# Performance work log

Measured on AMD Instinct MI355X. Metric: run time of the kernel, lower is better.

Reference implementation:

```python
import jax, jax.numpy as jnp
import numpy as np

BATCH, NUM_BSS, NUM_USERS, M, N = 32, 8, 32, 128, 4
LAGR_ITERS = 8
PSEUDOINV_SVAL_THRESH = 1e-12


def herm(a):
    return 0.5 * (a + jnp.swapaxes(a, -1, -2).conj())


def setup_inputs() -> dict:
    key = jax.random.key(0)
    ks = jax.random.split(key, 7)
    v_re = jax.random.normal(ks[0], (BATCH, NUM_USERS, M, N), jnp.float32)
    v_im = jax.random.normal(ks[1], (BATCH, NUM_USERS, M, N), jnp.float32)
    H_re = jax.random.normal(ks[2], (NUM_BSS, NUM_USERS, N, M), jnp.float32)
    H_im = jax.random.normal(ks[3], (NUM_BSS, NUM_USERS, N, M), jnp.float32)
    noise_pow = jax.random.uniform(ks[4], (BATCH, NUM_USERS), jnp.float32, 0.05, 1.0)
    rweights = jax.random.uniform(ks[5], (BATCH, NUM_USERS), jnp.float32, 0.1, 1.0)
    bss_pow = jnp.ones((BATCH, NUM_BSS), jnp.float32)
    assign = jax.random.randint(ks[6], (NUM_USERS,), 0, NUM_BSS).astype(jnp.int32)
    return {"v_re": v_re, "v_im": v_im, "H_re": H_re, "H_im": H_im,
            "noise_pow": noise_pow, "rweights": rweights, "bss_pow": bss_pow,
            "assign": assign}


def reference(v_re, v_im, H_re, H_im, noise_pow, rweights, bss_pow, assign):
    V = v_re + 1j * v_im          # [B,K,M,N] precoders
    H = H_re + 1j * H_im          # [C,K,N,M] channel BS c -> user k
    K = V.shape[1]
    C = H.shape[0]
    Ndim = V.shape[-1]
    eyeN = jnp.eye(Ndim, dtype=V.dtype)

    # Hg[j, i] = channel from assigned-BS-of-user-j to user i
    Hg = H[assign]                                    # [K,K,N,M]
    # downlink covariance per user i: noise*I + sum_j (H[bs_j,i] V_j)(.)^H
    HV = jnp.einsum('jinm,bjmp->bijnp', Hg, V)        # [B,Ki,Kj,N,N]
    cov = jnp.einsum('bijnp,bijqp->binq', HV, HV.conj())
    cov = herm(cov + noise_pow[..., None, None] * eyeN)
    icov = herm(jnp.linalg.inv(cov))                  # [B,K,N,N]

    idx = jnp.arange(K)
    Hd = Hg[idx, idx]                                 # [K,N,M] direct channels
    HdV = jnp.einsum('knm,bkmp->bknp', Hd, V)         # [B,K,N,N]
    u = jnp.einsum('bknq,bkqp->bknp', icov, HdV)      # receive filters
    w_inv = herm(eyeN - jnp.einsum('bkqn,bkqp->bknp', u.conj(), HdV))
    w = herm(jnp.linalg.inv(w_inv))                   # MSE weights (w_poly=None)
    uwu = herm(jnp.einsum('bknp,bkpq,bkrq->bknr', u, w, u.conj()))
    # v_tilde = H_ii^H u w * rate_weight
    vt = jnp.einsum('knm,bknp,bkpq->bkmq', Hd.conj(), u, w) * rweights[..., None, None]

    # uplink covariance per BS c: sum_k rw_k * H[c,k]^H uwu_k H[c,k]
    ul = herm(jnp.einsum('cknm,bkno,ckop,bk->bcmp', H.conj(), uwu, H, rweights))

    # aux per BS: sum over assigned users of v_tilde v_tilde^H
    Q = jnp.einsum('bkmn,bkpn->bkmp', vt, vt.conj())  # [B,K,M,M]
    aux = jnp.moveaxis(
        jax.ops.segment_sum(jnp.moveaxis(Q, 1, 0), assign, num_segments=C), 0, 1)  # [B,C,M,M]

    lam, E = jnp.linalg.eigh(ul)                      # [B,C,M], [B,C,M,M]
    lam = jnp.maximum(lam, 0.0)
    c = jnp.maximum(jnp.einsum('bcmi,bcmp,bcpi->bci', E.conj(), aux, E).real, 0.0)
    c = c / bss_pow[..., None]

    # solve sum_i c_i/(lam_i+mu)^2 = 1 for mu >= 0 by bisection in [0, sqrt(sum c)]
    hi = jnp.sqrt(jnp.sum(c, -1))
    lo = jnp.zeros_like(hi)
    for _ in range(LAGR_ITERS):
        mid = 0.5 * (lo + hi)
        f = jnp.sum(c / jnp.square(lam + mid[..., None] + 1e-20), -1)
        gt = f > 1.0
        lo = jnp.where(gt, mid, lo)
        hi = jnp.where(gt, hi, mid)
    mu = jnp.maximum(0.5 * (lo + hi), 0.0)            # [B,C]

    # pseudo-inverse of loaded UL covariance via its eigendecomposition
    lam_l = lam + mu[..., None]
    lam_l = jnp.where(lam_l < PSEUDOINV_SVAL_THRESH, 1e12, lam_l)
    inv_aug = herm(jnp.einsum('bcmi,bci,bcni->bcmn', E, 1.0 / lam_l, E.conj()))

    # v update: v_k = inv_aug[assign_k] @ v_tilde_k
    v_out = jnp.einsum('bkmp,bkpn->bkmn', inv_aug[:, assign], vt)  # [B,K,M,N]
    return v_out
```

## Files before the change

kernel.cpp:

```cpp
#include <hip/hip_runtime.h>

#define B_ 32
#define C_ 8
#define K_ 32
#define NCMAX 96
#define BSTR 129

__device__ __forceinline__ float2 cmul(float2 a, float2 b) {
  return make_float2(a.x*b.x - a.y*b.y, a.x*b.y + a.y*b.x);
}
__device__ __forceinline__ float2 cmulc(float2 a, float2 b) {
  return make_float2(a.x*b.x + a.y*b.y, a.y*b.x - a.x*b.y);
}
__device__ __forceinline__ float2 cadd(float2 a, float2 b){ return make_float2(a.x+b.x, a.y+b.y); }
__device__ __forceinline__ float2 csub(float2 a, float2 b){ return make_float2(a.x-b.x, a.y-b.y); }
__device__ __forceinline__ int SK(int r){ return r + ((r >> 3) << 1); }

__device__ void herm4_inv(float2 a[4][4], float2 out[4][4]) {
  float idg[4];
  for (int j = 0; j < 4; ++j) {
    float d = sqrtf(fmaxf(a[j][j].x, 1e-30f));
    float id = 1.f / d;
    idg[j] = id;
    a[j][j] = make_float2(d, 0.f);
    for (int r = j+1; r < 4; ++r) { a[r][j].x *= id; a[r][j].y *= id; }
    for (int c = j+1; c < 4; ++c)
      for (int r = c; r < 4; ++r)
        a[r][c] = csub(a[r][c], cmulc(a[r][j], a[c][j]));
  }
  float2 li[4][4];
  for (int j = 0; j < 4; ++j) {
    li[j][j] = make_float2(idg[j], 0.f);
    for (int r = j+1; r < 4; ++r) {
      float2 s = make_float2(0.f, 0.f);
      for (int d = j; d < r; ++d) s = cadd(s, cmul(a[r][d], li[d][j]));
      li[r][j] = make_float2(-s.x*idg[r], -s.y*idg[r]);
    }
  }
  for (int p = 0; p < 4; ++p)
    for (int q = 0; q < 4; ++q) {
      float2 s = make_float2(0.f, 0.f);
      for (int d = (p > q ? p : q); d < 4; ++d)
        s = cadd(s, cmulc(li[d][q], li[d][p]));
      out[p][q] = s;
    }
}

__global__ __launch_bounds__(512, 1) void k_fused(
    const float* __restrict__ v_re, const float* __restrict__ v_im,
    const float* __restrict__ H_re, const float* __restrict__ H_im,
    const float* __restrict__ noise_pow, const float* __restrict__ rweights,
    const float* __restrict__ bss_pow, const int* __restrict__ assign_g,
    void* __restrict__ outp, int omode)
{
  const int t = threadIdx.x;
  const int lane = t & 63, wid = t >> 6;
  const int blk = blockIdx.x;
  const int b = blk >> 3, c = blk & 7;
  const int tm = t >> 4, tp = t & 15;
  const int rbase = tm * 4, cbase = tp * 8;

  __shared__ __align__(16) float2 BsL[NCMAX * BSTR];
  __shared__ __align__(16) float2 Arena[4224];
  __shared__ __align__(16) float2 pS[1024];
  __shared__ __align__(16) float2 dBS2[256];
  __shared__ __align__(16) float2 wS[160];
  __shared__ __align__(16) float2 colS[160];
  __shared__ __align__(16) float2 pvS[128];
  __shared__ __align__(16) float2 tauS[128];
  __shared__ float dS[128], eS[128], cpS[128];
  __shared__ float red[8];
  __shared__ int asg[K_], ulist[K_], nc_s;

  float2* Wall = pS;
  float2* uwS  = pS + 512;
  float2* covS = Arena + 2576;
  float2* HdVS = Arena + 3088;
  float2* Pd   = Arena;
  float2* Tsc  = Arena;
  float2* Vp   = Arena;

  if (t < K_) asg[t] = assign_g[t];
  if (t == 0) {
    int n2 = 0;
    for (int k = 0; k < K_; ++k) if (assign_g[k] == c) ulist[n2++] = k;
    nc_s = n2;
  }
  {
    const int k = t >> 4, n = (t >> 2) & 3, q = t & 3;
    covS[t] = make_float2((n == q) ? noise_pow[b*K_ + k] : 0.f, 0.f);
  }
  __syncthreads();
  const int nc = nc_s;
  if (nc == 0) return;
  const int cols = 4 * nc;
  const int qmax = (cols + 15) >> 4;
  const int passes = (cols + 31) >> 5;

  {
    const int pn = t >> 2, qt = t & 3;
    const int kk = pn >> 2, nn = pn & 3;
    float2* Tb0 = Arena + 1552;
    float2* Tb1 = Arena + 2064;
    for (int j = 0; j < K_; j += 2) {
      #pragma unroll
      for (int bf = 0; bf < 2; ++bf) {
        const int vb = (b*K_ + j + bf) * 512;
        Arena[bf*776 + (t >> 2)*6 + (t & 3) + (t >> 7)*2] =
            make_float2(v_re[vb + t], v_im[vb + t]);
      }
      __syncthreads();
      float2 rr[2][4];
      #pragma unroll
      for (int bf = 0; bf < 2; ++bf) {
        const float2* Vq = Arena + bf*776 + qt*2;
        const int hb = ((asg[j + bf]*K_ + kk)*4 + nn) * 128;
        float2 a0 = {0,0}, a1 = {0,0}, a2 = {0,0}, a3 = {0,0};
        for (int m4 = qt*32; m4 < qt*32 + 32; m4 += 4) {
          const float4 hre = *(const float4*)&H_re[hb + m4];
          const float4 him = *(const float4*)&H_im[hb + m4];
          const float hx[4] = {hre.x, hre.y, hre.z, hre.w};
          const float hy[4] = {him.x, him.y, him.z, him.w};
          #pragma unroll
          for (int i2 = 0; i2 < 4; ++i2) {
            const float4 v01 = *(const float4*)&Vq[(m4 + i2)*6];
            const float4 v23 = *(const float4*)&Vq[(m4 + i2)*6 + 2];
            a0.x += hx[i2]*v01.x - hy[i2]*v01.y; a0.y += hx[i2]*v01.y + hy[i2]*v01.x;
            a1.x += hx[i2]*v01.z - hy[i2]*v01.w; a1.y += hx[i2]*v01.w + hy[i2]*v01.z;
            a2.x += hx[i2]*v23.x - hy[i2]*v23.y; a2.y += hx[i2]*v23.y + hy[i2]*v23.x;
            a3.x += hx[i2]*v23.z - hy[i2]*v23.w; a3.y += hx[i2]*v23.w + hy[i2]*v23.z;
          }
        }
        rr[bf][0] = a0; rr[bf][1] = a1; rr[bf][2] = a2; rr[bf][3] = a3;
      }
      #pragma unroll
      for (int o = 1; o <= 2; o <<= 1) {
        #pragma unroll
        for (int bf = 0; bf < 2; ++bf)
          #pragma unroll
          for (int p = 0; p < 4; ++p) {
            rr[bf][p].x += __shfl_xor(rr[bf][p].x, o, 64);
            rr[bf][p].y += __shfl_xor(rr[bf][p].y, o, 64);
          }
      }
      if (qt == 0) {
        #pragma unroll
        for (int p = 0; p < 4; ++p) {
          Tb0[pn*4 + p] = rr[0][p];
          Tb1[pn*4 + p] = rr[1][p];
        }
      }
      __syncthreads();
      {
        const int k2 = t >> 4, n2 = (t >> 2) & 3, q2 = t & 3;
        float2 acc = covS[t];
        #pragma unroll
        for (int p = 0; p < 4; ++p)
          acc = cadd(acc, cmulc(Tb0[(k2*4 + n2)*4 + p], Tb0[(k2*4 + q2)*4 + p]));
        #pragma unroll
        for (int p = 0; p < 4; ++p)
          acc = cadd(acc, cmulc(Tb1[(k2*4 + n2)*4 + p], Tb1[(k2*4 + q2)*4 + p]));
        covS[t] = acc;
        if (k2 == j)     HdVS[k2*16 + n2*4 + q2] = Tb0[(k2*4 + n2)*4 + q2];
        if (k2 == j + 1) HdVS[k2*16 + n2*4 + q2] = Tb1[(k2*4 + n2)*4 + q2];
      }
      __syncthreads();
    }
  }

  if (t < K_) {
    const int k = t;
    float2 a[4][4], ic[4][4], hv[4][4], u[4][4], wi[4][4], w[4][4], uw[4][4], W[4][4];
    const float rwk = rweights[b*K_ + k];
    for (int r = 0; r < 4; ++r)
      for (int c2 = 0; c2 < 4; ++c2) a[r][c2] = covS[k*16 + r*4 + c2];
    herm4_inv(a, ic);
    for (int r = 0; r < 4; ++r)
      for (int c2 = 0; c2 < 4; ++c2) hv[r][c2] = HdVS[k*16 + r*4 + c2];
    for (int n = 0; n < 4; ++n)
      for (int p = 0; p < 4; ++p) {
        float2 s = {0,0};
        for (int q = 0; q < 4; ++q) s = cadd(s, cmul(ic[n][q], hv[q][p]));
        u[n][p] = s;
      }
    for (int n = 0; n < 4; ++n)
      for (int p = 0; p < 4; ++p) {
        float2 s = make_float2((n == p) ? 1.f : 0.f, 0.f);
        for (int q = 0; q < 4; ++q) s = csub(s, cmulc(hv[q][p], u[q][n]));
        wi[n][p] = s;
      }
    herm4_inv(wi, w);
    for (int n = 0; n < 4; ++n)
      for (int q = 0; q < 4; ++q) {
        float2 s = {0,0};
        for (int p = 0; p < 4; ++p) s = cadd(s, cmul(u[n][p], w[p][q]));
        uw[n][q] = s;
      }
    for (int n = 0; n < 4; ++n)
      for (int r = 0; r < 4; ++r) {
        float2 s = {0,0};
        for (int q = 0; q < 4; ++q) s = cadd(s, cmulc(uw[n][q], u[r][q]));
        W[n][r] = make_float2(s.x * rwk, s.y * rwk);
      }
    for (int n = 0; n < 4; ++n)
      for (int r = n; r < 4; ++r) {
        float2 x1 = W[n][r], x2 = W[r][n];
        float2 hm = make_float2(0.5f*(x1.x + x2.x), 0.5f*(x1.y - x2.y));
        W[n][r] = hm; W[r][n] = make_float2(hm.x, -hm.y);
      }
    for (int idx = 0; idx < 16; ++idx) {
      uwS[k*16 + idx]  = uw[idx >> 2][idx & 3];
      Wall[k*16 + idx] = W[idx >> 2][idx & 3];
    }
  }
  __syncthreads();

  float2 Areg[4][8];
  #pragma unroll
  for (int j = 0; j < 4; ++j)
    #pragma unroll
    for (int cc = 0; cc < 8; ++cc) Areg[j][cc] = make_float2(0.f, 0.f);
  for (int k = 0; k < K_; k += 2) {
    #pragma unroll
    for (int bf = 0; bf < 2; ++bf) {
      const int hb = (c*K_ + k + bf) * 512;
      Arena[bf*520 + (t >> 7)*130 + (t & 127)] = make_float2(H_re[hb + t], H_im[hb + t]);
    }
    __syncthreads();
    #pragma unroll
    for (int bf = 0; bf < 2; ++bf) {
      const int n = t >> 7, p = t & 127;
      const float2* HsB = Arena + bf*520;
      const int kb = (k + bf)*16 + n*4;
      float2 y = {0,0};
      #pragma unroll
      for (int o = 0; o < 4; ++o) y = cadd(y, cmul(Wall[kb + o], HsB[o*130 + p]));
      Arena[1040 + bf*640 + n*160 + p + ((p >> 3) << 1)] = y;
    }
    __syncthreads();
    #pragma unroll
    for (int bf = 0; bf < 2; ++bf) {
      const float2* HsB = Arena + bf*520;
      const float2* YsB = Arena + 1040 + bf*640;
      #pragma unroll
      for (int n = 0; n < 4; ++n) {
        const float4 ha = *(const float4*)&HsB[n*130 + rbase];
        const float4 hc = *(const float4*)&HsB[n*130 + rbase + 2];
        const float2 h0 = make_float2(ha.x, ha.y), h1 = make_float2(ha.z, ha.w);
        const float2 h2 = make_float2(hc.x, hc.y), h3 = make_float2(hc.z, hc.w);
        const float2* yb = &YsB[n*160 + tp*10];
        #pragma unroll
        for (int hq = 0; hq < 2; ++hq) {
          float2 y[4];
          #pragma unroll
          for (int a2 = 0; a2 < 4; a2 += 2) {
            const float4 y4 = *(const float4*)&yb[hq*4 + a2];
            y[a2] = make_float2(y4.x, y4.y); y[a2+1] = make_float2(y4.z, y4.w);
          }
          #pragma unroll
          for (int c4 = 0; c4 < 4; ++c4) {
            const int cc = hq*4 + c4;
            Areg[0][cc].x += h0.x*y[c4].x + h0.y*y[c4].y;
            Areg[0][cc].y += h0.x*y[c4].y - h0.y*y[c4].x;
            Areg[1][cc].x += h1.x*y[c4].x + h1.y*y[c4].y;
            Areg[1][cc].y += h1.x*y[c4].y - h1.y*y[c4].x;
            Areg[2][cc].x += h2.x*y[c4].x + h2.y*y[c4].y;
            Areg[2][cc].y += h2.x*y[c4].y - h2.y*y[c4].x;
            Areg[3][cc].x += h3.x*y[c4].x + h3.y*y[c4].y;
            Areg[3][cc].y += h3.x*y[c4].y - h3.y*y[c4].x;
          }
        }
      }
    }
    __syncthreads();
  }

  float2 Bv[4][8];
  #pragma unroll
  for (int j = 0; j < 4; ++j)
    #pragma unroll
    for (int q = 0; q < 8; ++q) Bv[j][q] = make_float2(0.f, 0.f);
  float trp = 0.f;
  #pragma unroll
  for (int q = 0; q < 8; ++q) {
    const int col = tp + 16*q;
    const int slot = col >> 2, qn = col & 3;
    if (slot < nc) {
      const int k = ulist[slot];
      const float rwk = rweights[b*K_ + k];
      const int hb = (c*K_ + k) * 512;
      float2 acc0 = {0,0}, acc1 = {0,0}, acc2 = {0,0}, acc3 = {0,0};
      #pragma unroll
      for (int n = 0; n < 4; ++n) {
        const float2 uwv = uwS[k*16 + n*4 + qn];
        const float4 hre = *(const float4*)&H_re[hb + n*128 + rbase];
        const float4 him = *(const float4*)&H_im[hb + n*128 + rbase];
        acc0 = cadd(acc0, cmulc(uwv, make_float2(hre.x, him.x)));
        acc1 = cadd(acc1, cmulc(uwv, make_float2(hre.y, him.y)));
        acc2 = cadd(acc2, cmulc(uwv, make_float2(hre.z, him.z)));
        acc3 = cadd(acc3, cmulc(uwv, make_float2(hre.w, him.w)));
      }
      acc0.x *= rwk; acc0.y *= rwk; acc1.x *= rwk; acc1.y *= rwk;
      acc2.x *= rwk; acc2.y *= rwk; acc3.x *= rwk; acc3.y *= rwk;
      Bv[0][q] = acc0; Bv[1][q] = acc1; Bv[2][q] = acc2; Bv[3][q] = acc3;
      trp += acc0.x*acc0.x + acc0.y*acc0.y + acc1.x*acc1.x + acc1.y*acc1.y
           + acc2.x*acc2.x + acc2.y*acc2.y + acc3.x*acc3.x + acc3.y*acc3.y;
    }
  }
  #pragma unroll
  for (int o = 32; o >= 1; o >>= 1) trp += __shfl_xor(trp, o, 64);
  if (lane == 0) red[wid] = trp;
  __syncthreads();
  const float inv_bss = 1.f / bss_pow[b*C_ + c];
  float hi = sqrtf((red[0] + red[1] + red[2] + red[3] +
                    red[4] + red[5] + red[6] + red[7]) * inv_bss);
  float lo = 0.f;

  if (tp == 0) {
    #pragma unroll
    for (int j = 0; j < 4; ++j) colS[SK(rbase + j)] = Areg[j][0];
  }
  __syncthreads();

  #pragma unroll 1
  for (int i = 0; i < 127; ++i) {
    float2 vr[4], vc[8], tau, sc;
    {
      const float2 x0 = colS[SK(lane)], x1 = colS[SK(lane + 64)];
      float sig = 0.f;
      if (lane >= i + 2)      sig += x0.x*x0.x + x0.y*x0.y;
      if (lane + 64 >= i + 2) sig += x1.x*x1.x + x1.y*x1.y;
      #pragma unroll
      for (int o = 32; o >= 1; o >>= 1) sig += __shfl_xor(sig, o, 64);
      const float2 al = colS[SK(i + 1)];
      float beta;
      if (sig <= 1e-30f && fabsf(al.y) <= 1e-30f) {
        beta = al.x; tau = make_float2(0.f, 0.f); sc = make_float2(0.f, 0.f);
      } else {
        const float mag = sqrtf(al.x*al.x + al.y*al.y + sig);
        beta = (al.x >= 0.f) ? -mag : mag;
        const float ib = 1.f / beta;
        tau = make_float2((beta - al.x) * ib, -al.y * ib);
        const float dx = al.x - beta, dy = al.y;
        const float dn = 1.f / (dx*dx + dy*dy);
        sc = make_float2(dx*dn, -dy*dn);
      }
      if (t == 0) { eS[i] = beta; tauS[i] = tau; }
      #pragma unroll
      for (int j = 0; j < 4; ++j) {
        const int r = rbase + j;
        const float2 x = colS[SK(r)];
        vr[j] = (r <= i) ? make_float2(0.f, 0.f)
              : (r == i + 1 ? make_float2(1.f, 0.f) : cmul(x, sc));
      }
      {
        const int cb = SK(cbase);
        const float4 c01 = *(const float4*)&colS[cb];
        const float4 c23 = *(const float4*)&colS[cb + 2];
        const float4 c45 = *(const float4*)&colS[cb + 4];
        const float4 c67 = *(const float4*)&colS[cb + 6];
        const float2 cx[8] = { make_float2(c01.x,c01.y), make_float2(c01.z,c01.w),
                               make_float2(c23.x,c23.y), make_float2(c23.z,c23.w),
                               make_float2(c45.x,c45.y), make_float2(c45.z,c45.w),
                               make_float2(c67.x,c67.y), make_float2(c67.z,c67.w) };
        #pragma unroll
        for (int cc = 0; cc < 8; ++cc) {
          const int r = cbase + cc;
          vc[cc] = (r <= i) ? make_float2(0.f, 0.f)
                 : (r == i + 1 ? make_float2(1.f, 0.f) : cmul(cx[cc], sc));
        }
      }
    }
    {
      float2 part[4];
      #pragma unroll
      for (int j = 0; j < 4; ++j) {
        float2 s = cmul(Areg[j][0], vc[0]);
        #pragma unroll
        for (int cc = 1; cc < 8; ++cc) s = cadd(s, cmul(Areg[j][cc], vc[cc]));
        part[j] = s;
      }
      #pragma unroll
      for (int o = 1; o <= 8; o <<= 1) {
        #pragma unroll
        for (int j = 0; j < 4; ++j) {
          part[j].x += __shfl_xor(part[j].x, o, 64);
          part[j].y += __shfl_xor(part[j].y, o, 64);
        }
      }
      #pragma unroll
      for (int j = 0; j < 4; ++j) if (tp == j) pvS[rbase + j] = part[j];
      #pragma unroll
      for (int q = 0; q < 8; ++q) {
        if (q >= qmax) continue;
        float2 s = {0.f, 0.f};
        #pragma unroll
        for (int j = 0; j < 4; ++j) s = cadd(s, cmulc(Bv[j][q], vr[j]));
        Pd[tm*130 + tp + 16*q] = s;
      }
    }
    __syncthreads();

    if (wid == 0) {
      float2 p0 = {0.f,0.f}, p1 = {0.f,0.f};
      if (lane > i)      p0 = cmul(tau, pvS[lane]);
      if (lane + 64 > i) p1 = cmul(tau, pvS[lane + 64]);
      float2 v0, v1;
      v0 = (lane <= i) ? make_float2(0.f,0.f)
         : (lane == i + 1 ? make_float2(1.f,0.f) : cmul(colS[SK(lane)], sc));
      { const int r1 = lane + 64;
        v1 = (r1 <= i) ? make_float2(0.f,0.f)
           : (r1 == i + 1 ? make_float2(1.f,0.f) : cmul(colS[SK(r1)], sc)); }
      float2 d0 = cadd(cmulc(p0, v0), cmulc(p1, v1));
      #pragma unroll
      for (int o = 32; o >= 1; o >>= 1) {
        d0.x += __shfl_xor(d0.x, o, 64);
        d0.y += __shfl_xor(d0.y, o, 64);
      }
      const float alr = -0.5f * (tau.x*d0.x + tau.y*d0.y);
      wS[SK(lane)]      = cadd(p0, make_float2(alr*v0.x, alr*v0.y));
      wS[SK(lane + 64)] = cadd(p1, make_float2(alr*v1.x, alr*v1.y));
    } else if (t < 320) {
      const int col = (t - 64) & 127;
      const int half = (t - 64) >> 7;
      float2 s = {0.f, 0.f};
      #pragma unroll
      for (int g = 0; g < 16; ++g) s = cadd(s, Pd[(half*16 + g)*130 + col]);
      dBS2[half*128 + col] = s;
    }
    __syncthreads();

    {
      float2 wr[4], wc[8];
      #pragma unroll
      for (int j = 0; j < 4; ++j) wr[j] = wS[SK(rbase + j)];
      {
        const int cb = SK(cbase);
        const float4 w01 = *(const float4*)&wS[cb];
        const float4 w23 = *(const float4*)&wS[cb + 2];
        const float4 w45 = *(const float4*)&wS[cb + 4];
        const float4 w67 = *(const float4*)&wS[cb + 6];
        wc[0] = make_float2(w01.x,w01.y); wc[1] = make_float2(w01.z,w01.w);
        wc[2] = make_float2(w23.x,w23.y); wc[3] = make_float2(w23.z,w23.w);
        wc[4] = make_float2(w45.x,w45.y); wc[5] = make_float2(w45.z,w45.w);
        wc[6] = make_float2(w67.x,w67.y); wc[7] = make_float2(w67.z,w67.w);
      }
      #pragma unroll
      for (int j = 0; j < 4; ++j)
        #pragma unroll
        for (int cc = 0; cc < 8; ++cc)
          Areg[j][cc] = csub(Areg[j][cc], cadd(cmulc(vr[j], wc[cc]), cmulc(wr[j], vc[cc])));
      const float2 tauc = make_float2(tau.x, -tau.y);
      #pragma unroll
      for (int q = 0; q < 8; ++q) {
        if (q >= qmax) continue;
        const float2 dBt = cmul(tauc, cadd(dBS2[tp + 16*q], dBS2[128 + tp + 16*q]));
        #pragma unroll
        for (int j = 0; j < 4; ++j) Bv[j][q] = csub(Bv[j][q], cmul(dBt, vr[j]));
      }
      if (tp == (i >> 3)) {
        #pragma unroll
        for (int cc = 0; cc < 8; ++cc) if (cc == (i & 7)) {
          #pragma unroll
          for (int j = 0; j < 4; ++j) if (rbase + j >= i + 1) Areg[j][cc] = vr[j];
        }
      }
      if (tp == ((i + 1) >> 3)) {
        #pragma unroll
        for (int cc = 0; cc < 8; ++cc) if (cc == ((i + 1) & 7)) {
          #pragma unroll
          for (int j = 0; j < 4; ++j) colS[SK(rbase + j)] = Areg[j][cc];
        }
      }
    }
    __syncthreads();
  }

  if (tp == (tm >> 1)) {
    const int co = (tm & 1) * 4;
    #pragma unroll
    for (int j = 0; j < 4; ++j)
      #pragma unroll
      for (int cc = 0; cc < 8; ++cc)
        if (cc == co + j) dS[rbase + j] = Areg[j][cc].x;
  }
  #pragma unroll
  for (int q = 0; q < 8; ++q) {
    const int col = tp + 16*q;
    if ((col >> 2) < nc) {
      #pragma unroll
      for (int j = 0; j < 4; ++j) BsL[col*BSTR + rbase + j] = Bv[j][q];
    }
  }
  __syncthreads();

  if (wid == 0) {
    for (int it = 0; it <= 8; ++it) {
      const float mu = 0.5f * (lo + hi);
      float fsum = 0.f;
      for (int p = 0; p < passes; ++p) {
        const int colg = 32*p + (lane & 31);
        const bool act = (lane < 32) && (colg < cols);
        float2* Bcol = BsL + colg*BSTR;
        float m = dS[0] + mu;
        float im = 1.f / m;
        float2 g = act ? Bcol[0] : make_float2(0.f, 0.f);
        g.x *= im; g.y *= im;
        if (act) Tsc[lane] = g;
        float cp = eS[0] * im;
        if (lane == 0) cpS[0] = cp;
        for (int r = 1; r < 128; ++r) {
          const float e0 = eS[r-1];
          m = dS[r] + mu - e0 * cp;
          im = 1.f / m;
          float2 gr = act ? Bcol[r] : make_float2(0.f, 0.f);
          gr.x = (gr.x - e0 * g.x) * im;
          gr.y = (gr.y - e0 * g.y) * im;
          g = gr;
          if (act) Tsc[r*33 + lane] = gr;
          if (r < 127) { cp = eS[r] * im; if (lane == 0) cpS[r] = cp; }
        }
        float2 z = g;
        float acc = z.x*z.x + z.y*z.y;
        if (it == 8 && act) Bcol[127] = z;
        for (int r = 126; r >= 0; --r) {
          const float cpr = cpS[r];
          const float2 gp = act ? Tsc[r*33 + lane] : make_float2(0.f, 0.f);
          z.x = gp.x - cpr * z.x;
          z.y = gp.y - cpr * z.y;
          acc += z.x*z.x + z.y*z.y;
          if (it == 8 && act) Bcol[r] = z;
        }
        if (act) fsum += acc;
      }
      if (it < 8) {
        #pragma unroll
        for (int o = 32; o >= 1; o >>= 1) fsum += __shfl_xor(fsum, o, 64);
        const float f = fsum * inv_bss;
        if (f > 1.0f) lo = mu; else hi = mu;
      }
    }
  }
  __syncthreads();

  for (int base = 0; base < cols; base += 32) {
    float2 z0[4], z1[4];
    bool act[4];
    #pragma unroll
    for (int qq = 0; qq < 4; ++qq) {
      const int col = base + wid + 8*qq;
      act[qq] = (col < cols);
      const int cc2 = act[qq] ? col : 0;
      z0[qq] = BsL[cc2*BSTR + lane];
      z1[qq] = BsL[cc2*BSTR + lane + 64];
    }
    for (int P = 7; P >= 0; --P) {
      const int p0i = P * 16;
      const int smax = (P == 7) ? 14 : 15;
      __syncthreads();
      if (tp == 2*P) {
        #pragma unroll
        for (int s = 0; s < 8; ++s) {
          const int ii = p0i + s;
          #pragma unroll
          for (int j = 0; j < 4; ++j) {
            const int r = rbase + j;
            Vp[(s << 7) + r] = (r >= ii + 1) ? Areg[j][s] : make_float2(0.f, 0.f);
          }
        }
      }
      if (tp == 2*P + 1) {
        #pragma unroll
        for (int s = 8; s < 16; ++s) {
          if (s > smax) continue;
          const int ii = p0i + s;
          #pragma unroll
          for (int j = 0; j < 4; ++j) {
            const int r = rbase + j;
            Vp[(s << 7) + r] = (r >= ii + 1) ? Areg[j][s - 8] : make_float2(0.f, 0.f);
          }
        }
      }
      __syncthreads();
      for (int s = smax; s >= 0; --s) {
        const float2 tv = tauS[p0i + s];
        const float2 v0 = Vp[(s << 7) + lane];
        const float2 v1 = Vp[(s << 7) + lane + 64];
        float2 d[4];
        #pragma unroll
        for (int qq = 0; qq < 4; ++qq)
          d[qq] = cadd(cmulc(z0[qq], v0), cmulc(z1[qq], v1));
        #pragma unroll
        for (int o = 32; o >= 1; o >>= 1) {
          #pragma unroll
          for (int qq = 0; qq < 4; ++qq) {
            d[qq].x += __shfl_xor(d[qq].x, o, 64);
            d[qq].y += __shfl_xor(d[qq].y, o, 64);
          }
        }
        #pragma unroll
        for (int qq = 0; qq < 4; ++qq) {
          const float2 td = cmul(tv, d[qq]);
          z0[qq] = csub(z0[qq], cmul(td, v0));
          z1[qq] = csub(z1[qq], cmul(td, v1));
        }
      }
    }
    #pragma unroll
    for (int qq = 0; qq < 4; ++qq) if (act[qq]) {
      const int col = base + wid + 8*qq;
      const int slotc = col >> 2, qn = col & 3;
      const int k = ulist[slotc];
      const size_t obase = (size_t)(b*K_ + k) * 512;
      const size_t oe0 = obase + (size_t)lane*4 + qn;
      const size_t oe1 = obase + (size_t)(lane + 64)*4 + qn;
      if (omode == 0) {
        ((float2*)outp)[oe0] = z0[qq];
        ((float2*)outp)[oe1] = z1[qq];
      } else {
        ((float*)outp)[oe0] = z0[qq].x;
        ((float*)outp)[oe1] = z1[qq].x;
      }
    }
  }
}

extern "C" void kernel_launch(void* const* d_in, const int* in_sizes, int n_in,
                              void* d_out, int out_size, void* d_ws, size_t ws_size,
                              hipStream_t stream)
{
  (void)in_sizes; (void)n_in; (void)d_ws; (void)ws_size;
  const float* v_re   = (const float*)d_in[0];
  const float* v_im   = (const float*)d_in[1];
  const float* H_re   = (const float*)d_in[2];
  const float* H_im   = (const float*)d_in[3];
  const float* noise  = (const float*)d_in[4];
  const float* rw     = (const float*)d_in[5];
  const float* bss    = (const float*)d_in[6];
  const int*   assign = (const int*)d_in[7];

  const int omode = (out_size == B_*K_*128*4) ? 1 : 0;

  hipLaunchKernelGGL(k_fused, dim3(B_*C_), dim3(512), 0, stream,
                     v_re, v_im, H_re, H_im, noise, rw, bss, assign, d_out, omode);
}
```

Before: 1.354 ms.

## Defer Householder rank-2 update to next iteration, dropping one barrier per step

The Householder tridiagonalization loop is restructured so the rank-2 trailing update of the register-held matrix and the B update from step i run at the start of step i+1. The next pivot column is computed directly by wave 0 from a raw column copy plus the new v and w vectors, instead of being extracted after the full update. This removes one __syncthreads per iteration across 127 iterations. In exchange it adds a vLds buffer, a colRaw buffer and some shuffles, and the column correction must exactly match the deferred update.

```diff
diff --git a/kernel.cpp b/kernel.cpp
--- a/kernel.cpp
+++ b/kernel.cpp
@@ -65,7 +65,9 @@
   __shared__ __align__(16) float2 pS[1024];
   __shared__ __align__(16) float2 dBS2[256];
   __shared__ __align__(16) float2 wS[160];
+  __shared__ __align__(16) float2 vLds[160];
   __shared__ __align__(16) float2 colS[160];
+  __shared__ __align__(16) float2 colRaw[128];
   __shared__ __align__(16) float2 pvS[128];
   __shared__ __align__(16) float2 tauS[128];
   __shared__ float dS[128], eS[128], cpS[128];
@@ -322,8 +324,58 @@
   }
   __syncthreads();
 
+  float2 tau_p = make_float2(0.f, 0.f);
+
   #pragma unroll 1
   for (int i = 0; i < 127; ++i) {
+    if (i > 0) {
+      const int ip = i - 1;
+      float2 vr4[4], wr4[4], vc4[8], wc4[8];
+      #pragma unroll
+      for (int j = 0; j < 4; ++j) {
+        vr4[j] = vLds[SK(rbase + j)];
+        wr4[j] = wS[SK(rbase + j)];
+      }
+      {
+        const int cb = SK(cbase);
+        const float4 v01 = *(const float4*)&vLds[cb];
+        const float4 v23 = *(const float4*)&vLds[cb + 2];
+        const float4 v45 = *(const float4*)&vLds[cb + 4];
+        const float4 v67 = *(const float4*)&vLds[cb + 6];
+        vc4[0] = make_float2(v01.x,v01.y); vc4[1] = make_float2(v01.z,v01.w);
+        vc4[2] = make_float2(v23.x,v23.y); vc4[3] = make_float2(v23.z,v23.w);
+        vc4[4] = make_float2(v45.x,v45.y); vc4[5] = make_float2(v45.z,v45.w);
+        vc4[6] = make_float2(v67.x,v67.y); vc4[7] = make_float2(v67.z,v67.w);
+        const float4 w01 = *(const float4*)&wS[cb];
+        const float4 w23 = *(const float4*)&wS[cb + 2];
+        const float4 w45 = *(const float4*)&wS[cb + 4];
+        const float4 w67 = *(const float4*)&wS[cb + 6];
+        wc4[0] = make_float2(w01.x,w01.y); wc4[1] = make_float2(w01.z,w01.w);
+        wc4[2] = make_float2(w23.x,w23.y); wc4[3] = make_float2(w23.z,w23.w);
+        wc4[4] = make_float2(w45.x,w45.y); wc4[5] = make_float2(w45.z,w45.w);
+        wc4[6] = make_float2(w67.x,w67.y); wc4[7] = make_float2(w67.z,w67.w);
+      }
+      #pragma unroll
+      for (int j = 0; j < 4; ++j)
+        #pragma unroll
+        for (int cc = 0; cc < 8; ++cc)
+          Areg[j][cc] = csub(Areg[j][cc], cadd(cmulc(vr4[j], wc4[cc]), cmulc(wr4[j], vc4[cc])));
+      const float2 tauc = make_float2(tau_p.x, -tau_p.y);
+      #pragma unroll
+      for (int q = 0; q < 8; ++q) {
+        if (q >= qmax) continue;
+        const float2 dBt = cmul(tauc, cadd(dBS2[tp + 16*q], dBS2[128 + tp + 16*q]));
+        #pragma unroll
+        for (int j = 0; j < 4; ++j) Bv[j][q] = csub(Bv[j][q], cmul(dBt, vr4[j]));
+      }
+      if (tp == (ip >> 3)) {
+        #pragma unroll
+        for (int cc = 0; cc < 8; ++cc) if (cc == (ip & 7)) {
+          #pragma unroll
+          for (int j = 0; j < 4; ++j) if (rbase + j >= ip + 1) Areg[j][cc] = vr4[j];
+        }
+      }
+    }
     float2 vr[4], vc[8], tau, sc;
     {
       const float2 x0 = colS[SK(lane)], x1 = colS[SK(lane + 64)];
@@ -398,6 +450,13 @@
         for (int j = 0; j < 4; ++j) s = cadd(s, cmulc(Bv[j][q], vr[j]));
         Pd[tm*130 + tp + 16*q] = s;
       }
+      if (tp == ((i + 1) >> 3)) {
+        #pragma unroll
+        for (int cc = 0; cc < 8; ++cc) if (cc == ((i + 1) & 7)) {
+          #pragma unroll
+          for (int j = 0; j < 4; ++j) colRaw[rbase + j] = Areg[j][cc];
+        }
+      }
     }
     __syncthreads();
 
@@ -418,8 +477,19 @@
         d0.y += __shfl_xor(d0.y, o, 64);
       }
       const float alr = -0.5f * (tau.x*d0.x + tau.y*d0.y);
-      wS[SK(lane)]      = cadd(p0, make_float2(alr*v0.x, alr*v0.y));
-      wS[SK(lane + 64)] = cadd(p1, make_float2(alr*v1.x, alr*v1.y));
+      const float2 w0 = cadd(p0, make_float2(alr*v0.x, alr*v0.y));
+      const float2 w1 = cadd(p1, make_float2(alr*v1.x, alr*v1.y));
+      wS[SK(lane)]      = w0;
+      wS[SK(lane + 64)] = w1;
+      vLds[SK(lane)]      = v0;
+      vLds[SK(lane + 64)] = v1;
+      const int rs = (i + 1) & 63;
+      const float bx0 = __shfl(w0.x, rs, 64), by0 = __shfl(w0.y, rs, 64);
+      const float bx1 = __shfl(w1.x, rs, 64), by1 = __shfl(w1.y, rs, 64);
+      const float2 wb = (i + 1 < 64) ? make_float2(bx0, by0) : make_float2(bx1, by1);
+      const float2 c0 = colRaw[lane], c1 = colRaw[lane + 64];
+      colS[SK(lane)]      = csub(csub(c0, cmulc(v0, wb)), w0);
+      colS[SK(lane + 64)] = csub(csub(c1, cmulc(v1, wb)), w1);
     } else if (t < 320) {
       const int col = (t - 64) & 127;
       const int half = (t - 64) >> 7;
@@ -429,51 +499,56 @@
       dBS2[half*128 + col] = s;
     }
     __syncthreads();
-
+    tau_p = tau;
+  }
+
+  {
+    const int ip = 126;
+    float2 vr4[4], wr4[4], vc4[8], wc4[8];
+    #pragma unroll
+    for (int j = 0; j < 4; ++j) {
+      vr4[j] = vLds[SK(rbase + j)];
+      wr4[j] = wS[SK(rbase + j)];
+    }
     {
-      float2 wr[4], wc[8];
-      #pragma unroll
-      for (int j = 0; j < 4; ++j) wr[j] = wS[SK(rbase + j)];
-      {
-        const int cb = SK(cbase);
-        const float4 w01 = *(const float4*)&wS[cb];
-        const float4 w23 = *(const float4*)&wS[cb + 2];
-        const float4 w45 = *(const float4*)&wS[cb + 4];
-        const float4 w67 = *(const float4*)&wS[cb + 6];
-        wc[0] = make_float2(w01.x,w01.y); wc[1] = make_float2(w01.z,w01.w);
-        wc[2] = make_float2(w23.x,w23.y); wc[3] = make_float2(w23.z,w23.w);
-        wc[4] = make_float2(w45.x,w45.y); wc[5] = make_float2(w45.z,w45.w);
-        wc[6] = make_float2(w67.x,w67.y); wc[7] = make_float2(w67.z,w67.w);
-      }
-      #pragma unroll
-      for (int j = 0; j < 4; ++j)
-        #pragma unroll
-        for (int cc = 0; cc < 8; ++cc)
-          Areg[j][cc] = csub(Areg[j][cc], cadd(cmulc(vr[j], wc[cc]), cmulc(wr[j], vc[cc])));
-      const float2 tauc = make_float2(tau.x, -tau.y);
-      #pragma unroll
-      for (int q = 0; q < 8; ++q) {
-        if (q >= qmax) continue;
-        const float2 dBt = cmul(tauc, cadd(dBS2[tp + 16*q], dBS2[128 + tp + 16*q]));
-        #pragma unroll
-        for (int j = 0; j < 4; ++j) Bv[j][q] = csub(Bv[j][q], cmul(dBt, vr[j]));
-      }
-      if (tp == (i >> 3)) {
-        #pragma unroll
-        for (int cc = 0; cc < 8; ++cc) if (cc == (i & 7)) {
-          #pragma unroll
-          for (int j = 0; j < 4; ++j) if (rbase + j >= i + 1) Areg[j][cc] = vr[j];
-        }
-      }
-      if (tp == ((i + 1) >> 3)) {
-        #pragma unroll
-        for (int cc = 0; cc < 8; ++cc) if (cc == ((i + 1) & 7)) {
-          #pragma unroll
-          for (int j = 0; j < 4; ++j) colS[SK(rbase + j)] = Areg[j][cc];
-        }
-      }
-    }
-    __syncthreads();
+      const int cb = SK(cbase);
+      const float4 v01 = *(const float4*)&vLds[cb];
+      const float4 v23 = *(const float4*)&vLds[cb + 2];
+      const float4 v45 = *(const float4*)&vLds[cb + 4];
+      const float4 v67 = *(const float4*)&vLds[cb + 6];
+      vc4[0] = make_float2(v01.x,v01.y); vc4[1] = make_float2(v01.z,v01.w);
+      vc4[2] = make_float2(v23.x,v23.y); vc4[3] = make_float2(v23.z,v23.w);
+      vc4[4] = make_float2(v45.x,v45.y); vc4[5] = make_float2(v45.z,v45.w);
+      vc4[6] = make_float2(v67.x,v67.y); vc4[7] = make_float2(v67.z,v67.w);
+      const float4 w01 = *(const float4*)&wS[cb];
+      const float4 w23 = *(const float4*)&wS[cb + 2];
+      const float4 w45 = *(const float4*)&wS[cb + 4];
+      const float4 w67 = *(const float4*)&wS[cb + 6];
+      wc4[0] = make_float2(w01.x,w01.y); wc4[1] = make_float2(w01.z,w01.w);
+      wc4[2] = make_float2(w23.x,w23.y); wc4[3] = make_float2(w23.z,w23.w);
+      wc4[4] = make_float2(w45.x,w45.y); wc4[5] = make_float2(w45.z,w45.w);
+      wc4[6] = make_float2(w67.x,w67.y); wc4[7] = make_float2(w67.z,w67.w);
+    }
+    #pragma unroll
+    for (int j = 0; j < 4; ++j)
+      #pragma unroll
+      for (int cc = 0; cc < 8; ++cc)
+        Areg[j][cc] = csub(Areg[j][cc], cadd(cmulc(vr4[j], wc4[cc]), cmulc(wr4[j], vc4[cc])));
+    const float2 tauc = make_float2(tau_p.x, -tau_p.y);
+    #pragma unroll
+    for (int q = 0; q < 8; ++q) {
+      if (q >= qmax) continue;
+      const float2 dBt = cmul(tauc, cadd(dBS2[tp + 16*q], dBS2[128 + tp + 16*q]));
+      #pragma unroll
+      for (int j = 0; j < 4; ++j) Bv[j][q] = csub(Bv[j][q], cmul(dBt, vr4[j]));
+    }
+    if (tp == (ip >> 3)) {
+      #pragma unroll
+      for (int cc = 0; cc < 8; ++cc) if (cc == (ip & 7)) {
+        #pragma unroll
+        for (int j = 0; j < 4; ++j) if (rbase + j >= ip + 1) Areg[j][cc] = vr4[j];
+      }
+    }
   }
 
   if (tp == (tm >> 1)) {
```

After: 1.365 ms. No clear change (+0.8%).
